# Kernel optimization log

Hardware: AMD Instinct MI355X
Metric: run time of the kernel (lower is better)

Reference implementation:

```python
import jax, jax.numpy as jnp
import numpy as np

B, S, D = 4, 4096, 64

def setup_inputs() -> dict:
    key = jax.random.key(0)
    k1, k2 = jax.random.split(key)
    query = jax.random.normal(k1, (B, S, D), dtype=jnp.float32)
    value = jax.random.normal(k2, (B, S, D), dtype=jnp.float32)
    return {"query": query, "value": value}

def reference(query, value):
    # score = Q @ V^T  -> [B, Sq, Skv]  (note: value acts as both key and value; no 1/sqrt(d) scaling)
    score = jnp.einsum("bqd,bkd->bqk", query, value)
    attn_weights = jax.nn.softmax(score, axis=-1)
    context = jnp.einsum("bqk,bkd->bqd", attn_weights, value)
    return (context, attn_weights)
```

## Files before the change

### kernel.cpp

```cpp
#include <hip/hip_runtime.h>

#define BB 4
#define SS 4096
#define DD 64
#define NSLOT 128
#define SLOTB 12288
#define IMGB ((size_t)NSLOT * SLOTB)
#define KS 4

typedef _Float16 h16;
typedef h16 half2_t __attribute__((ext_vector_type(2)));
typedef h16 half8_t __attribute__((ext_vector_type(8)));
typedef float f32x2 __attribute__((ext_vector_type(2)));
typedef float f32x4 __attribute__((ext_vector_type(4)));
typedef float f32x16 __attribute__((ext_vector_type(16)));
typedef unsigned u32x4v __attribute__((ext_vector_type(4)));

#define Z16 ((f32x16){0.f,0.f,0.f,0.f,0.f,0.f,0.f,0.f,0.f,0.f,0.f,0.f,0.f,0.f,0.f,0.f})

__device__ __forceinline__ unsigned pkh(float a, float b) {
    half2_t x = {(h16)a, (h16)b};
    return __builtin_bit_cast(unsigned, x);
}

__device__ __forceinline__ void xpair(unsigned& wl, unsigned& wh, int h) {
    unsigned xl = (unsigned)__shfl_xor((int)wl, 32);
    unsigned xh = (unsigned)__shfl_xor((int)wh, 32);
    unsigned nl = h ? xh : wl;
    unsigned nh = h ? wh : xl;
    wl = nl; wh = nh;
}

__global__ __launch_bounds__(512) void prep_v(const float* __restrict__ V,
                                              char* __restrict__ W) {
    const int t    = threadIdx.x;
    const int slot = blockIdx.x;
    const int b    = blockIdx.y;
    char* img = W + (size_t)b * IMGB + (size_t)slot * SLOTB;
    const float* Vb = V + (size_t)b * SS * DD;
    if (t < 256) {
        const int s    = t >> 6;
        const int lane = t & 63;
        const int kr   = lane & 31, h = lane >> 5;
        const float* src = Vb + (size_t)(slot * 32 + kr) * DD + s * 16 + h * 8;
        f32x4 a = *(const f32x4*)src;
        f32x4 c = *(const f32x4*)(src + 4);
        half8_t hi, lo;
#pragma unroll
        for (int j = 0; j < 4; ++j) {
            float x = a[j]; h16 hh = (h16)x;
            hi[j] = hh; lo[j] = (h16)(x - (float)hh);
            float y = c[j]; h16 gg = (h16)y;
            hi[j + 4] = gg; lo[j + 4] = (h16)(y - (float)gg);
        }
        *(half8_t*)(img + s * 2048 + lane * 16) = hi;
        *(half8_t*)(img + s * 2048 + 1024 + lane * 16) = lo;
    } else {
        const int u    = t - 256;
        const int ks   = u >> 7;
        const int o    = (u >> 6) & 1;
        const int lane = u & 63;
        const int kr   = lane & 31, h = lane >> 5;
        const int d    = o * 32 + kr;
        half8_t v;
#pragma unroll
        for (int j = 0; j < 8; ++j)
            v[j] = (h16)Vb[(size_t)(slot * 32 + ks * 16 + h * 8 + j) * DD + d];
        *(half8_t*)(img + 8192 + ks * 2048 + o * 1024 + lane * 16) = v;
    }
}

__device__ __forceinline__ f32x16 scores12(const char* sb, const half8_t* qh,
                                           const half8_t* ql, int lane) {
    f32x16 sa = Z16, sc = Z16;
#pragma unroll
    for (int s = 0; s < 4; ++s) {
        half8_t ah = *(const half8_t*)(sb + s * 2048 + lane * 16);
        half8_t al = *(const half8_t*)(sb + s * 2048 + 1024 + lane * 16);
        if (s & 1) {
            sc = __builtin_amdgcn_mfma_f32_32x32x16_f16(ah, qh[s], sc, 0, 0, 0);
            sc = __builtin_amdgcn_mfma_f32_32x32x16_f16(ah, ql[s], sc, 0, 0, 0);
            sc = __builtin_amdgcn_mfma_f32_32x32x16_f16(al, qh[s], sc, 0, 0, 0);
        } else {
            sa = __builtin_amdgcn_mfma_f32_32x32x16_f16(ah, qh[s], sa, 0, 0, 0);
            sa = __builtin_amdgcn_mfma_f32_32x32x16_f16(ah, ql[s], sa, 0, 0, 0);
            sa = __builtin_amdgcn_mfma_f32_32x32x16_f16(al, qh[s], sa, 0, 0, 0);
        }
    }
    return sa + sc;
}

__device__ __forceinline__ void load_q(const float* Qrow, half8_t* qh, half8_t* ql) {
#pragma unroll
    for (int s = 0; s < 4; ++s) {
        f32x4 a = *(const f32x4*)(Qrow + s * 16);
        (void)a;
    }
}

__device__ __forceinline__ void qfrags(const float* Qrow, int h, half8_t* qh, half8_t* ql) {
#pragma unroll
    for (int s = 0; s < 4; ++s) {
        f32x4 a = *(const f32x4*)(Qrow + s * 16 + h * 8);
        f32x4 c = *(const f32x4*)(Qrow + s * 16 + h * 8 + 4);
#pragma unroll
        for (int j = 0; j < 4; ++j) {
            float x = a[j]; h16 hh = (h16)x;
            qh[s][j] = hh; ql[s][j] = (h16)(x - (float)hh);
            float y = c[j]; h16 gg = (h16)y;
            qh[s][j + 4] = gg; ql[s][j + 4] = (h16)(y - (float)gg);
        }
    }
}

__global__ __launch_bounds__(512, 4) void stats_pass(const float* __restrict__ Q,
                                                     const char* __restrict__ W,
                                                     f32x2* __restrict__ ml) {
    const int t    = threadIdx.x;
    const int wid  = t >> 6;
    const int lane = t & 63;
    const int kr   = lane & 31, h = lane >> 5;
    const int bid  = blockIdx.x;
    const int b    = bid & 3;
    const int u    = (bid >> 2) * 8 + wid;
    const int qgb  = u >> 2;
    const int kspl = u & 3;
    const char* img = W + (size_t)b * IMGB;
    const float* Qrow = Q + ((size_t)b * SS + qgb * 32 + kr) * DD;

    half8_t qh[4], ql[4];
    qfrags(Qrow, h, qh, ql);

    float mrun = -1e30f, lrun = 0.f;
#pragma unroll 2
    for (int slot = kspl * 32; slot < kspl * 32 + 32; ++slot) {
        f32x16 sc = scores12(img + (size_t)slot * SLOTB, qh, ql, lane);
        float tmax = sc[0];
#pragma unroll
        for (int i = 1; i < 16; ++i) tmax = fmaxf(tmax, sc[i]);
        tmax = fmaxf(tmax, __shfl_xor(tmax, 32));
        const float mn = fmaxf(mrun, tmax);
        float ps = 0.f;
#pragma unroll
        for (int i = 0; i < 16; ++i) ps += __expf(sc[i] - mn);
        ps += __shfl_xor(ps, 32);
        const bool still  = __all(tmax <= mrun);
        const float alpha = still ? 1.f : __expf(mrun - mn);
        lrun = lrun * alpha + ps;
        mrun = mn;
    }
    if (h == 0)
        ml[((size_t)b * SS + qgb * 32 + kr) * KS + kspl] = (f32x2){mrun, lrun};
}

__global__ __launch_bounds__(512, 4) void attn_pass(const float* __restrict__ Q,
                                                    const char* __restrict__ W,
                                                    const f32x2* __restrict__ ml,
                                                    float* __restrict__ ctx,
                                                    float* __restrict__ attn) {
    __shared__ float red[8][32][66];
    const int t    = threadIdx.x;
    const int wid  = t >> 6;
    const int lane = t & 63;
    const int kr   = lane & 31, h = lane >> 5;
    const int bid  = blockIdx.x;
    const int b    = bid & 3;
    const int qgb  = bid >> 2;
    const size_t row = (size_t)b * SS + qgb * 32 + kr;
    const char* img = W + (size_t)b * IMGB;

    f32x2 s0 = ml[row * KS + 0], s1 = ml[row * KS + 1];
    f32x2 s2 = ml[row * KS + 2], s3 = ml[row * KS + 3];
    float mg = fmaxf(fmaxf(s0[0], s1[0]), fmaxf(s2[0], s3[0]));
    float lg = s0[1] * __expf(s0[0] - mg) + s1[1] * __expf(s1[0] - mg) +
               s2[1] * __expf(s2[0] - mg) + s3[1] * __expf(s3[0] - mg);
    const float moff = mg + __logf(lg);

    half8_t qh[4], ql[4];
    qfrags(Q + row * DD, h, qh, ql);

    f32x16 oc0 = Z16, oc1 = Z16;
    float* arow = attn + row * SS;

#pragma unroll 1
    for (int i = 0; i < 16; ++i) {
        const int slot = wid * 16 + i;
        const char* sb = img + (size_t)slot * SLOTB;
        f32x16 sc = scores12(sb, qh, ql, lane);
        float p[16];
#pragma unroll
        for (int j = 0; j < 16; ++j) p[j] = __expf(sc[j] - moff);
#pragma unroll
        for (int g = 0; g < 4; ++g) {
            f32x4 wv = {p[g * 4], p[g * 4 + 1], p[g * 4 + 2], p[g * 4 + 3]};
            *(f32x4*)&arow[slot * 32 + g * 8 + h * 4] = wv;
        }
        unsigned w0 = pkh(p[0], p[1]),   w1 = pkh(p[2], p[3]);
        unsigned w2 = pkh(p[4], p[5]),   w3 = pkh(p[6], p[7]);
        unsigned w4 = pkh(p[8], p[9]),   w5 = pkh(p[10], p[11]);
        unsigned w6 = pkh(p[12], p[13]), w7 = pkh(p[14], p[15]);
        xpair(w0, w2, h); xpair(w1, w3, h); xpair(w4, w6, h); xpair(w5, w7, h);
        half8_t pb0 = __builtin_bit_cast(half8_t, (u32x4v){w0, w1, w2, w3});
        half8_t pb1 = __builtin_bit_cast(half8_t, (u32x4v){w4, w5, w6, w7});
#pragma unroll
        for (int ks = 0; ks < 2; ++ks) {
            const half8_t bp = ks ? pb1 : pb0;
            half8_t av0 = *(const half8_t*)(sb + 8192 + ks * 2048 + lane * 16);
            half8_t av1 = *(const half8_t*)(sb + 8192 + ks * 2048 + 1024 + lane * 16);
            oc0 = __builtin_amdgcn_mfma_f32_32x32x16_f16(av0, bp, oc0, 0, 0, 0);
            oc1 = __builtin_amdgcn_mfma_f32_32x32x16_f16(av1, bp, oc1, 0, 0, 0);
        }
    }

#pragma unroll
    for (int g = 0; g < 4; ++g) {
        f32x4 a = {oc0[g * 4], oc0[g * 4 + 1], oc0[g * 4 + 2], oc0[g * 4 + 3]};
        f32x4 c = {oc1[g * 4], oc1[g * 4 + 1], oc1[g * 4 + 2], oc1[g * 4 + 3]};
        *(f32x4*)&red[wid][kr][g * 8 + h * 4]      = a;
        *(f32x4*)&red[wid][kr][32 + g * 8 + h * 4] = c;
    }
    __syncthreads();
    const int q = t >> 4, c16 = t & 15;
    f32x4 sum = {0.f, 0.f, 0.f, 0.f};
#pragma unroll
    for (int w2 = 0; w2 < 8; ++w2) sum += *(const f32x4*)&red[w2][q][c16 * 4];
    *(f32x4*)&ctx[((size_t)b * SS + qgb * 32 + q) * DD + c16 * 4] = sum;
}

extern "C" void kernel_launch(void* const* d_in, const int* in_sizes, int n_in,
                              void* d_out, int out_size, void* d_ws, size_t ws_size,
                              hipStream_t stream) {
    const float* Q = (const float*)d_in[0];
    const float* V = (const float*)d_in[1];
    float* ctx  = (float*)d_out;
    float* attn = (float*)d_out + (size_t)BB * SS * DD;
    char*  W  = (char*)d_ws;
    f32x2* ml = (f32x2*)(W + BB * IMGB);
    prep_v<<<dim3(NSLOT, BB), 512, 0, stream>>>(V, W);
    stats_pass<<<dim3(256), 512, 0, stream>>>(Q, W, ml);
    attn_pass<<<dim3(512), 512, 0, stream>>>(Q, W, ml, ctx, attn);
}
```

Baseline: 372.7 us.

## Share V fragments across two query tiles in stats pass and stage attn stores via LDS

The stats pass now gives each wave two 32-row query tiles, so every loaded V fragment feeds both tiles' MFMAs. Blocks shrink to 256 threads while the grid stays the same size. In the attention pass, each wave transposes its 32x32 probability tile through a swizzled LDS buffer, so global attn writes go out as contiguous row segments instead of scattered float4 stores. This costs extra registers for the second query fragment set, some LDS traffic, and reuse of the reduction buffer behind a barrier.

Result: faster. 353.7 us (-5.1%).

```diff
diff --git a/kernel.cpp b/kernel.cpp
--- a/kernel.cpp
+++ b/kernel.cpp
@@ -70,6 +70,37 @@
     }
 }
 
+__device__ __forceinline__ void qfrags(const float* Qrow, int h, half8_t* qh, half8_t* ql) {
+#pragma unroll
+    for (int s = 0; s < 4; ++s) {
+        f32x4 a = *(const f32x4*)(Qrow + s * 16 + h * 8);
+        f32x4 c = *(const f32x4*)(Qrow + s * 16 + h * 8 + 4);
+#pragma unroll
+        for (int j = 0; j < 4; ++j) {
+            float x = a[j]; h16 hh = (h16)x;
+            qh[s][j] = hh; ql[s][j] = (h16)(x - (float)hh);
+            float y = c[j]; h16 gg = (h16)y;
+            qh[s][j + 4] = gg; ql[s][j + 4] = (h16)(y - (float)gg);
+        }
+    }
+}
+
+__device__ __forceinline__ void ml_update(const f32x16& sc, float& mrun, float& lrun) {
+    float tmax = sc[0];
+#pragma unroll
+    for (int i = 1; i < 16; ++i) tmax = fmaxf(tmax, sc[i]);
+    tmax = fmaxf(tmax, __shfl_xor(tmax, 32));
+    const float mn = fmaxf(mrun, tmax);
+    float ps = 0.f;
+#pragma unroll
+    for (int i = 0; i < 16; ++i) ps += __expf(sc[i] - mn);
+    ps += __shfl_xor(ps, 32);
+    const bool still  = __all(tmax <= mrun);
+    const float alpha = still ? 1.f : __expf(mrun - mn);
+    lrun = lrun * alpha + ps;
+    mrun = mn;
+}
+
 __device__ __forceinline__ f32x16 scores12(const char* sb, const half8_t* qh,
                                            const half8_t* ql, int lane) {
     f32x16 sa = Z16, sc = Z16;
@@ -90,30 +121,7 @@
     return sa + sc;
 }
 
-__device__ __forceinline__ void load_q(const float* Qrow, half8_t* qh, half8_t* ql) {
-#pragma unroll
-    for (int s = 0; s < 4; ++s) {
-        f32x4 a = *(const f32x4*)(Qrow + s * 16);
-        (void)a;
-    }
-}
-
-__device__ __forceinline__ void qfrags(const float* Qrow, int h, half8_t* qh, half8_t* ql) {
-#pragma unroll
-    for (int s = 0; s < 4; ++s) {
-        f32x4 a = *(const f32x4*)(Qrow + s * 16 + h * 8);
-        f32x4 c = *(const f32x4*)(Qrow + s * 16 + h * 8 + 4);
-#pragma unroll
-        for (int j = 0; j < 4; ++j) {
-            float x = a[j]; h16 hh = (h16)x;
-            qh[s][j] = hh; ql[s][j] = (h16)(x - (float)hh);
-            float y = c[j]; h16 gg = (h16)y;
-            qh[s][j + 4] = gg; ql[s][j + 4] = (h16)(y - (float)gg);
-        }
-    }
-}
-
-__global__ __launch_bounds__(512, 4) void stats_pass(const float* __restrict__ Q,
+__global__ __launch_bounds__(256, 4) void stats_pass(const float* __restrict__ Q,
                                                      const char* __restrict__ W,
                                                      f32x2* __restrict__ ml) {
     const int t    = threadIdx.x;
@@ -122,35 +130,40 @@
     const int kr   = lane & 31, h = lane >> 5;
     const int bid  = blockIdx.x;
     const int b    = bid & 3;
-    const int u    = (bid >> 2) * 8 + wid;
-    const int qgb  = u >> 2;
-    const int kspl = u & 3;
+    const int job  = (bid >> 2) * 4 + wid;
+    const int qp   = job >> 2;
+    const int kspl = job & 3;
     const char* img = W + (size_t)b * IMGB;
-    const float* Qrow = Q + ((size_t)b * SS + qgb * 32 + kr) * DD;
-
-    half8_t qh[4], ql[4];
-    qfrags(Qrow, h, qh, ql);
-
-    float mrun = -1e30f, lrun = 0.f;
-#pragma unroll 2
+    const size_t q0row = (size_t)b * SS + qp * 64 + kr;
+    const size_t q1row = q0row + 32;
+
+    half8_t qh0[4], ql0[4], qh1[4], ql1[4];
+    qfrags(Q + q0row * DD, h, qh0, ql0);
+    qfrags(Q + q1row * DD, h, qh1, ql1);
+
+    float m0 = -1e30f, l0 = 0.f, m1 = -1e30f, l1 = 0.f;
+#pragma unroll 1
     for (int slot = kspl * 32; slot < kspl * 32 + 32; ++slot) {
-        f32x16 sc = scores12(img + (size_t)slot * SLOTB, qh, ql, lane);
-        float tmax = sc[0];
-#pragma unroll
-        for (int i = 1; i < 16; ++i) tmax = fmaxf(tmax, sc[i]);
-        tmax = fmaxf(tmax, __shfl_xor(tmax, 32));
-        const float mn = fmaxf(mrun, tmax);
-        float ps = 0.f;
-#pragma unroll
-        for (int i = 0; i < 16; ++i) ps += __expf(sc[i] - mn);
-        ps += __shfl_xor(ps, 32);
-        const bool still  = __all(tmax <= mrun);
-        const float alpha = still ? 1.f : __expf(mrun - mn);
-        lrun = lrun * alpha + ps;
-        mrun = mn;
-    }
-    if (h == 0)
-        ml[((size_t)b * SS + qgb * 32 + kr) * KS + kspl] = (f32x2){mrun, lrun};
+        const char* sb = img + (size_t)slot * SLOTB;
+        f32x16 s0 = Z16, s1 = Z16;
+#pragma unroll
+        for (int s = 0; s < 4; ++s) {
+            half8_t ah = *(const half8_t*)(sb + s * 2048 + lane * 16);
+            half8_t al = *(const half8_t*)(sb + s * 2048 + 1024 + lane * 16);
+            s0 = __builtin_amdgcn_mfma_f32_32x32x16_f16(ah, qh0[s], s0, 0, 0, 0);
+            s1 = __builtin_amdgcn_mfma_f32_32x32x16_f16(ah, qh1[s], s1, 0, 0, 0);
+            s0 = __builtin_amdgcn_mfma_f32_32x32x16_f16(ah, ql0[s], s0, 0, 0, 0);
+            s1 = __builtin_amdgcn_mfma_f32_32x32x16_f16(ah, ql1[s], s1, 0, 0, 0);
+            s0 = __builtin_amdgcn_mfma_f32_32x32x16_f16(al, qh0[s], s0, 0, 0, 0);
+            s1 = __builtin_amdgcn_mfma_f32_32x32x16_f16(al, qh1[s], s1, 0, 0, 0);
+        }
+        ml_update(s0, m0, l0);
+        ml_update(s1, m1, l1);
+    }
+    if (h == 0) {
+        ml[q0row * KS + kspl] = (f32x2){m0, l0};
+        ml[q1row * KS + kspl] = (f32x2){m1, l1};
+    }
 }
 
 __global__ __launch_bounds__(512, 4) void attn_pass(const float* __restrict__ Q,
@@ -158,7 +171,7 @@
                                                     const f32x2* __restrict__ ml,
                                                     float* __restrict__ ctx,
                                                     float* __restrict__ attn) {
-    __shared__ float red[8][32][66];
+    __shared__ float LB[16896];
     const int t    = threadIdx.x;
     const int wid  = t >> 6;
     const int lane = t & 63;
@@ -168,6 +181,7 @@
     const int qgb  = bid >> 2;
     const size_t row = (size_t)b * SS + qgb * 32 + kr;
     const char* img = W + (size_t)b * IMGB;
+    float* tile = LB + wid * 1024;
 
     f32x2 s0 = ml[row * KS + 0], s1 = ml[row * KS + 1];
     f32x2 s2 = ml[row * KS + 2], s3 = ml[row * KS + 3];
@@ -180,7 +194,7 @@
     qfrags(Q + row * DD, h, qh, ql);
 
     f32x16 oc0 = Z16, oc1 = Z16;
-    float* arow = attn + row * SS;
+    float* aBase = attn + ((size_t)b * SS + qgb * 32) * SS;
 
 #pragma unroll 1
     for (int i = 0; i < 16; ++i) {
@@ -190,11 +204,21 @@
         float p[16];
 #pragma unroll
         for (int j = 0; j < 16; ++j) p[j] = __expf(sc[j] - moff);
+
 #pragma unroll
         for (int g = 0; g < 4; ++g) {
             f32x4 wv = {p[g * 4], p[g * 4 + 1], p[g * 4 + 2], p[g * 4 + 3]};
-            *(f32x4*)&arow[slot * 32 + g * 8 + h * 4] = wv;
-        }
+            const int chunk = (2 * g + h) ^ (kr & 7);
+            *(f32x4*)&tile[kr * 32 + chunk * 4] = wv;
+        }
+#pragma unroll
+        for (int j = 0; j < 4; ++j) {
+            const int rrow = j * 8 + (lane >> 3);
+            const int cc   = lane & 7;
+            f32x4 v = *(const f32x4*)&tile[rrow * 32 + ((cc ^ (rrow & 7)) * 4)];
+            *(f32x4*)&aBase[(size_t)rrow * SS + slot * 32 + cc * 4] = v;
+        }
+
         unsigned w0 = pkh(p[0], p[1]),   w1 = pkh(p[2], p[3]);
         unsigned w2 = pkh(p[4], p[5]),   w3 = pkh(p[6], p[7]);
         unsigned w4 = pkh(p[8], p[9]),   w5 = pkh(p[10], p[11]);
@@ -212,6 +236,8 @@
         }
     }
 
+    __syncthreads();
+    float (*red)[32][66] = (float(*)[32][66])LB;
 #pragma unroll
     for (int g = 0; g < 4; ++g) {
         f32x4 a = {oc0[g * 4], oc0[g * 4 + 1], oc0[g * 4 + 2], oc0[g * 4 + 3]};
@@ -237,6 +263,6 @@
     char*  W  = (char*)d_ws;
     f32x2* ml = (f32x2*)(W + BB * IMGB);
     prep_v<<<dim3(NSLOT, BB), 512, 0, stream>>>(V, W);
-    stats_pass<<<dim3(256), 512, 0, stream>>>(Q, W, ml);
+    stats_pass<<<dim3(256), 256, 0, stream>>>(Q, W, ml);
     attn_pass<<<dim3(512), 512, 0, stream>>>(Q, W, ml, ctx, attn);
 }
```
